# Kernel optimization log

Measured on AMD Instinct MI355X. Metric: run time of the kernel, lower is better.

The kernel has to match this reference:

```python
import jax, jax.numpy as jnp
import numpy as np

ALPHA = 0.01  # LeakyReLU negative slope
NEG_INF = -1e30


def setup_inputs() -> dict:
    key = jax.random.key(0)
    ks = jax.random.split(key, 8)
    B, N, F_IN, F_OUT, H = 4, 512, 256, 128, 64
    x_text = jax.random.normal(ks[0], (B, N, F_IN), dtype=jnp.float32)
    adj = jax.random.randint(ks[1], (B, N, N), 0, 2).astype(jnp.float32)
    # W: Linear(in_features, out_features)
    W = jax.random.normal(ks[2], (F_OUT, F_IN), dtype=jnp.float32) * (1.0 / np.sqrt(F_IN))
    bW = jnp.zeros((F_OUT,), dtype=jnp.float32)
    # afcs: Linear(2*out, hidden) -> ReLU -> Linear(hidden, 1)
    A1 = jax.random.normal(ks[3], (H, 2 * F_OUT), dtype=jnp.float32) * (1.0 / np.sqrt(2 * F_OUT))
    b1 = jnp.zeros((H,), dtype=jnp.float32)
    A2 = jax.random.normal(ks[4], (1, H), dtype=jnp.float32) * (1.0 / np.sqrt(H))
    b2 = jnp.zeros((1,), dtype=jnp.float32)
    return {"x_text": x_text, "adj": adj, "W": W, "bW": bW, "A1": A1, "b1": b1, "A2": A2, "b2": b2}


def reference(x_text, adj, W, bW, A1, b1, A2, b2):
    B, N, _ = x_text.shape
    F_OUT = W.shape[0]
    h = jnp.einsum('bnf,of->bno', x_text, W) + bW  # [B,N,F_OUT]
    # Split first MLP layer: A1 @ concat(h_i, h_j) = A1a h_i + A1b h_j
    A1a, A1b = A1[:, :F_OUT], A1[:, F_OUT:]
    hi = jnp.einsum('bno,ho->bnh', h, A1a)  # contribution of source node i
    hj = jnp.einsum('bno,ho->bnh', h, A1b)  # contribution of target node j
    z = jax.nn.relu(hi[:, :, None, :] + hj[:, None, :, :] + b1)  # [B,N,N,H]
    e = jnp.einsum('bijh,h->bij', z, A2[0]) + b2[0]              # [B,N,N]
    e = jnp.where(e >= 0, e, ALPHA * e)  # LeakyReLU
    logits = e * adj + (1.0 - adj) * NEG_INF  # mask_logits
    # NOTE: original softmax is over the flattened N*N axis per batch element
    attn = jax.nn.softmax(logits.reshape(B, N * N), axis=1).reshape(B, N, N)
    feature = jnp.einsum('bij,bjo->bio', attn, h)  # bmm aggregate
    return jax.nn.elu(feature)  # concat=True
```

## Files before the change

kernel.cpp:

```cpp
#include <hip/hip_runtime.h>
#include <math.h>

#define BB 4
#define NN 512
#define F_IN 256
#define F_OUT 128
#define HH 64
#define NEG_INF_F -1e30f
#define LALPHA 0.01f

typedef float f32x2 __attribute__((ext_vector_type(2)));

__global__ __launch_bounds__(512) void k_proj(
    const float* __restrict__ x, const float* __restrict__ W,
    const float* __restrict__ bW, const float* __restrict__ A1,
    const float* __restrict__ b1,
    float* __restrict__ h, float* __restrict__ hi, float* __restrict__ hjP)
{
    const int row0 = blockIdx.x * 8;
    const int b    = row0 >> 9;
    const int nl0  = row0 & 511;
    const int tid  = threadIdx.x;

    __shared__ float xs[8 * F_IN];
    __shared__ float hs[8 * F_OUT];
    __shared__ float hjs[8 * HH];
    __shared__ float red[4][8][F_OUT];

    #pragma unroll
    for (int t = 0; t < 4; ++t)
        xs[tid + t * 512] = x[(size_t)row0 * F_IN + tid + t * 512];
    __syncthreads();

    {
        const int o  = tid & 127;
        const int kq = tid >> 7;
        float acc[8] = {0, 0, 0, 0, 0, 0, 0, 0};
        const float4* wr = (const float4*)(W + (size_t)o * F_IN + kq * 64);
        #pragma unroll 4
        for (int it = 0; it < 16; ++it) {
            const float4 wv = wr[it];
            #pragma unroll
            for (int r = 0; r < 8; ++r) {
                const float4 xv = *((const float4*)(xs + r * F_IN + kq * 64) + it);
                acc[r] = fmaf(xv.x, wv.x, acc[r]);
                acc[r] = fmaf(xv.y, wv.y, acc[r]);
                acc[r] = fmaf(xv.z, wv.z, acc[r]);
                acc[r] = fmaf(xv.w, wv.w, acc[r]);
            }
        }
        #pragma unroll
        for (int r = 0; r < 8; ++r) red[kq][r][o] = acc[r];
    }
    __syncthreads();
    #pragma unroll
    for (int t = 0; t < 2; ++t) {
        const int idx = tid + t * 512;
        const int r = idx >> 7, o = idx & 127;
        const float v = red[0][r][o] + red[1][r][o] + red[2][r][o] + red[3][r][o] + bW[o];
        h[((size_t)row0 + r) * F_OUT + o] = v;
        hs[r * F_OUT + o] = v;
    }
    __syncthreads();

    {
        const int kh2  = tid & 127;
        const int k    = kh2 & 63, half = kh2 >> 6;
        const int oq   = tid >> 7;
        float acc[8] = {0, 0, 0, 0, 0, 0, 0, 0};
        const float4* ar = (const float4*)(A1 + (size_t)k * (2 * F_OUT) + half * F_OUT + oq * 32);
        #pragma unroll
        for (int it = 0; it < 8; ++it) {
            const float4 av = ar[it];
            #pragma unroll
            for (int r = 0; r < 8; ++r) {
                const float4 hv = *((const float4*)(hs + r * F_OUT + oq * 32) + it);
                acc[r] = fmaf(hv.x, av.x, acc[r]);
                acc[r] = fmaf(hv.y, av.y, acc[r]);
                acc[r] = fmaf(hv.z, av.z, acc[r]);
                acc[r] = fmaf(hv.w, av.w, acc[r]);
            }
        }
        __syncthreads();
        #pragma unroll
        for (int r = 0; r < 8; ++r) red[oq][r][kh2] = acc[r];
    }
    __syncthreads();
    #pragma unroll
    for (int t = 0; t < 2; ++t) {
        const int idx = tid + t * 512;
        const int r = idx >> 7, kh2 = idx & 127;
        const float v = red[0][r][kh2] + red[1][r][kh2] + red[2][r][kh2] + red[3][r][kh2];
        if (kh2 < 64) hi[((size_t)row0 + r) * HH + kh2] = v + b1[kh2];
        else          hjs[r * HH + (kh2 - 64)] = v;
    }
    __syncthreads();
    if (tid < 128) {
        const int k4 = tid >> 3, rr = tid & 7;
        float4 v;
        v.x = hjs[rr * HH + k4 * 4 + 0];
        v.y = hjs[rr * HH + k4 * 4 + 1];
        v.z = hjs[rr * HH + k4 * 4 + 2];
        v.w = hjs[rr * HH + k4 * 4 + 3];
        *(float4*)(hjP + (((size_t)b * 16 + k4) * NN + nl0 + rr) * 4) = v;
    }
}

__global__ __launch_bounds__(512, 2) void k_score_agg(
    const float* __restrict__ hi, const float* __restrict__ hjP,
    const float* __restrict__ A2, const float* __restrict__ b2,
    const float* __restrict__ adj, const float* __restrict__ h,
    float* __restrict__ y, float* __restrict__ stat_m, float* __restrict__ stat_s)
{
    const int blk   = blockIdx.x;
    const int b     = blk >> 7;
    const int itile = (blk >> 1) & 63;
    const int jh    = blk & 1;
    const int i0    = itile * 8;
    const int tid   = threadIdx.x;
    const int jt    = tid & 255;
    const int j     = jh * 256 + jt;

    __shared__ float a2s[HH];
    __shared__ float e_lds[256][12];
    __shared__ float red[4][8][F_OUT];
    __shared__ float rtmp[16];

    if (tid < HH) a2s[tid] = A2[tid];
    __syncthreads();

    float4 hjr[16];
    const float4* hjp = (const float4*)hjP + (size_t)b * 16 * NN + j;
    #pragma unroll
    for (int k4 = 0; k4 < 16; ++k4) hjr[k4] = hjp[(size_t)k4 * NN];

    const int rowu = __builtin_amdgcn_readfirstlane(b * NN + i0 + (tid >> 8) * 4);
    const float* hrow = hi + (size_t)rowu * HH;

    const f32x2 z2 = {0.0f, 0.0f};
    f32x2 s2[4] = {z2, z2, z2, z2};
    #pragma unroll
    for (int k4 = 0; k4 < 16; ++k4) {
        const f32x2 a2lo = *(const f32x2*)(a2s + k4 * 4);
        const f32x2 a2hi = *(const f32x2*)(a2s + k4 * 4 + 2);
        const f32x2 hjlo = {hjr[k4].x, hjr[k4].y};
        const f32x2 hjhi = {hjr[k4].z, hjr[k4].w};
        #pragma unroll
        for (int r = 0; r < 4; ++r) {
            const float* hp = hrow + r * HH + k4 * 4;
            const f32x2 hlo = {hp[0], hp[1]};
            const f32x2 hhi = {hp[2], hp[3]};
            s2[r] = __builtin_elementwise_fma(
                        __builtin_elementwise_max(hlo + hjlo, z2), a2lo, s2[r]);
            s2[r] = __builtin_elementwise_fma(
                        __builtin_elementwise_max(hhi + hjhi, z2), a2hi, s2[r]);
        }
    }
    float s4[4];
    #pragma unroll
    for (int r = 0; r < 4; ++r) s4[r] = s2[r].x + s2[r].y;

    const float b2v = b2[0];
    const int rh = tid >> 8;
    float lmax = -INFINITY;
    #pragma unroll
    for (int r = 0; r < 4; ++r) {
        float v = s4[r] + b2v;
        v = (v >= 0.0f) ? v : LALPHA * v;
        const float a = adj[((size_t)b * NN + i0 + rh * 4 + r) * NN + j];
        v = (a != 0.0f) ? v : NEG_INF_F;
        s4[r] = v;
        lmax = fmaxf(lmax, v);
    }

    #pragma unroll
    for (int off = 32; off; off >>= 1) lmax = fmaxf(lmax, __shfl_xor(lmax, off, 64));
    if ((tid & 63) == 0) rtmp[tid >> 6] = lmax;
    __syncthreads();
    float m_blk = rtmp[0];
    #pragma unroll
    for (int w = 1; w < 8; ++w) m_blk = fmaxf(m_blk, rtmp[w]);

    float4 w4;
    w4.x = __expf(s4[0] - m_blk);
    w4.y = __expf(s4[1] - m_blk);
    w4.z = __expf(s4[2] - m_blk);
    w4.w = __expf(s4[3] - m_blk);
    *(float4*)(&e_lds[jt][rh * 4]) = w4;
    float ls = w4.x + w4.y + w4.z + w4.w;
    #pragma unroll
    for (int off = 32; off; off >>= 1) ls += __shfl_xor(ls, off, 64);
    if ((tid & 63) == 0) rtmp[8 + (tid >> 6)] = ls;
    __syncthreads();
    if (tid == 0) {
        stat_m[blk] = m_blk;
        float ssum = 0.0f;
        #pragma unroll
        for (int w = 0; w < 8; ++w) ssum += rtmp[8 + w];
        stat_s[blk] = ssum;
    }

    {
        const int o = tid & 127;
        const int p = tid >> 7;
        f32x2 acc2[4] = {z2, z2, z2, z2};
        const float* hb = h + (size_t)b * NN * F_OUT;
        #pragma unroll 4
        for (int q = 0; q < 64; ++q) {
            const int jl = p * 64 + q;
            const float hv = hb[(size_t)(jh * 256 + jl) * F_OUT + o];
            const f32x2 hv2 = {hv, hv};
            const f32x2 wa = *(const f32x2*)&e_lds[jl][0];
            const f32x2 wb = *(const f32x2*)&e_lds[jl][2];
            const f32x2 wc = *(const f32x2*)&e_lds[jl][4];
            const f32x2 wd = *(const f32x2*)&e_lds[jl][6];
            acc2[0] = __builtin_elementwise_fma(wa, hv2, acc2[0]);
            acc2[1] = __builtin_elementwise_fma(wb, hv2, acc2[1]);
            acc2[2] = __builtin_elementwise_fma(wc, hv2, acc2[2]);
            acc2[3] = __builtin_elementwise_fma(wd, hv2, acc2[3]);
        }
        #pragma unroll
        for (int c = 0; c < 4; ++c) {
            red[p][2 * c + 0][o] = acc2[c].x;
            red[p][2 * c + 1][o] = acc2[c].y;
        }
    }
    __syncthreads();
    #pragma unroll
    for (int t = 0; t < 2; ++t) {
        const int idx = tid + t * 512;
        const int r = idx >> 7, oo = idx & 127;
        y[(size_t)blk * 1024 + idx] =
            red[0][r][oo] + red[1][r][oo] + red[2][r][oo] + red[3][r][oo];
    }
}

__global__ __launch_bounds__(256) void k_finish(
    const float* __restrict__ y, const float* __restrict__ stat_m,
    const float* __restrict__ stat_s, float* __restrict__ out)
{
    const int blk   = blockIdx.x;
    const int b     = blk >> 6;
    const int itile = blk & 63;
    const int tid   = threadIdx.x;

    __shared__ float sm[4], ss[4];

    const float m = (tid < 128) ? stat_m[b * 128 + tid] : -INFINITY;
    float lm = m;
    #pragma unroll
    for (int off = 32; off; off >>= 1) lm = fmaxf(lm, __shfl_xor(lm, off, 64));
    if ((tid & 63) == 0) sm[tid >> 6] = lm;
    __syncthreads();
    const float M = fmaxf(fmaxf(sm[0], sm[1]), fmaxf(sm[2], sm[3]));

    float sv = (tid < 128) ? stat_s[b * 128 + tid] * expf(m - M) : 0.0f;
    #pragma unroll
    for (int off = 32; off; off >>= 1) sv += __shfl_xor(sv, off, 64);
    if ((tid & 63) == 0) ss[tid >> 6] = sv;
    __syncthreads();
    const float invS = 1.0f / (ss[0] + ss[1] + ss[2] + ss[3]);

    const float sc0 = expf(stat_m[b * 128 + itile * 2 + 0] - M) * invS;
    const float sc1 = expf(stat_m[b * 128 + itile * 2 + 1] - M) * invS;
    const float4* y04 = (const float4*)(y + (size_t)(b * 128 + itile * 2 + 0) * 1024);
    const float4* y14 = (const float4*)(y + (size_t)(b * 128 + itile * 2 + 1) * 1024);
    float4* ob4 = (float4*)(out + ((size_t)b * NN + itile * 8) * F_OUT);

    const float4 v0 = y04[tid];
    const float4 v1 = y14[tid];
    float4 vv;
    vv.x = v0.x * sc0 + v1.x * sc1;
    vv.y = v0.y * sc0 + v1.y * sc1;
    vv.z = v0.z * sc0 + v1.z * sc1;
    vv.w = v0.w * sc0 + v1.w * sc1;
    vv.x = (vv.x > 0.0f) ? vv.x : expm1f(vv.x);
    vv.y = (vv.y > 0.0f) ? vv.y : expm1f(vv.y);
    vv.z = (vv.z > 0.0f) ? vv.z : expm1f(vv.z);
    vv.w = (vv.w > 0.0f) ? vv.w : expm1f(vv.w);
    ob4[tid] = vv;
}

extern "C" void kernel_launch(void* const* d_in, const int* in_sizes, int n_in,
                              void* d_out, int out_size, void* d_ws, size_t ws_size,
                              hipStream_t stream) {
    const float* x   = (const float*)d_in[0];
    const float* adj = (const float*)d_in[1];
    const float* W   = (const float*)d_in[2];
    const float* bW  = (const float*)d_in[3];
    const float* A1  = (const float*)d_in[4];
    const float* b1  = (const float*)d_in[5];
    const float* A2  = (const float*)d_in[6];
    const float* b2  = (const float*)d_in[7];
    float* out = (float*)d_out;

    float* ws = (float*)d_ws;
    float* h      = ws;
    float* hi     = h   + (size_t)BB * NN * F_OUT;
    float* hjP    = hi  + (size_t)BB * NN * HH;
    float* y      = hjP + (size_t)BB * HH * NN;
    float* stat_m = y   + (size_t)512 * 1024;
    float* stat_s = stat_m + 512;

    k_proj     <<<BB * 64,  512, 0, stream>>>(x, W, bW, A1, b1, h, hi, hjP);
    k_score_agg<<<BB * 128, 512, 0, stream>>>(hi, hjP, A2, b2, adj, h, y, stat_m, stat_s);
    k_finish   <<<BB * 64,  256, 0, stream>>>(y, stat_m, stat_s, out);
}
```

Before: 33.47 us.

## Process full j range per score block, halving grid and partial outputs

Each score/aggregate block now covers all 512 target nodes for an 8-row tile instead of splitting j into two halves. Each thread computes 8 rows of scores rather than 4, and aggregation loops over 128 j per group. This halves the partial y buffer and the softmax stats, and simplifies the finish kernel to a single-wave stat reduction with no block syncs. The cost is fewer blocks (256 rather than 512) on a large GPU, more registers per thread and dropped occupancy hint, plus a longer serial aggregation loop.

```diff
diff --git a/kernel.cpp b/kernel.cpp
--- a/kernel.cpp
+++ b/kernel.cpp
@@ -106,23 +106,21 @@
     }
 }
 
-__global__ __launch_bounds__(512, 2) void k_score_agg(
+__global__ __launch_bounds__(512) void k_score_agg(
     const float* __restrict__ hi, const float* __restrict__ hjP,
     const float* __restrict__ A2, const float* __restrict__ b2,
     const float* __restrict__ adj, const float* __restrict__ h,
     float* __restrict__ y, float* __restrict__ stat_m, float* __restrict__ stat_s)
 {
     const int blk   = blockIdx.x;
-    const int b     = blk >> 7;
-    const int itile = (blk >> 1) & 63;
-    const int jh    = blk & 1;
+    const int b     = blk >> 6;
+    const int itile = blk & 63;
     const int i0    = itile * 8;
     const int tid   = threadIdx.x;
-    const int jt    = tid & 255;
-    const int j     = jh * 256 + jt;
+    const int j     = tid;
 
     __shared__ float a2s[HH];
-    __shared__ float e_lds[256][12];
+    __shared__ float e_lds[NN][12];
     __shared__ float red[4][8][F_OUT];
     __shared__ float rtmp[16];
 
@@ -134,11 +132,11 @@
     #pragma unroll
     for (int k4 = 0; k4 < 16; ++k4) hjr[k4] = hjp[(size_t)k4 * NN];
 
-    const int rowu = __builtin_amdgcn_readfirstlane(b * NN + i0 + (tid >> 8) * 4);
+    const int rowu = __builtin_amdgcn_readfirstlane(b * NN + i0);
     const float* hrow = hi + (size_t)rowu * HH;
 
     const f32x2 z2 = {0.0f, 0.0f};
-    f32x2 s2[4] = {z2, z2, z2, z2};
+    f32x2 s2[8] = {z2, z2, z2, z2, z2, z2, z2, z2};
     #pragma unroll
     for (int k4 = 0; k4 < 16; ++k4) {
         const f32x2 a2lo = *(const f32x2*)(a2s + k4 * 4);
@@ -146,7 +144,7 @@
         const f32x2 hjlo = {hjr[k4].x, hjr[k4].y};
         const f32x2 hjhi = {hjr[k4].z, hjr[k4].w};
         #pragma unroll
-        for (int r = 0; r < 4; ++r) {
+        for (int r = 0; r < 8; ++r) {
             const float* hp = hrow + r * HH + k4 * 4;
             const f32x2 hlo = {hp[0], hp[1]};
             const f32x2 hhi = {hp[2], hp[3]};
@@ -156,20 +154,19 @@
                         __builtin_elementwise_max(hhi + hjhi, z2), a2hi, s2[r]);
         }
     }
-    float s4[4];
-    #pragma unroll
-    for (int r = 0; r < 4; ++r) s4[r] = s2[r].x + s2[r].y;
+    float s8[8];
+    #pragma unroll
+    for (int r = 0; r < 8; ++r) s8[r] = s2[r].x + s2[r].y;
 
     const float b2v = b2[0];
-    const int rh = tid >> 8;
     float lmax = -INFINITY;
     #pragma unroll
-    for (int r = 0; r < 4; ++r) {
-        float v = s4[r] + b2v;
+    for (int r = 0; r < 8; ++r) {
+        float v = s8[r] + b2v;
         v = (v >= 0.0f) ? v : LALPHA * v;
-        const float a = adj[((size_t)b * NN + i0 + rh * 4 + r) * NN + j];
+        const float a = adj[((size_t)b * NN + i0 + r) * NN + j];
         v = (a != 0.0f) ? v : NEG_INF_F;
-        s4[r] = v;
+        s8[r] = v;
         lmax = fmaxf(lmax, v);
     }
 
@@ -181,13 +178,18 @@
     #pragma unroll
     for (int w = 1; w < 8; ++w) m_blk = fmaxf(m_blk, rtmp[w]);
 
-    float4 w4;
-    w4.x = __expf(s4[0] - m_blk);
-    w4.y = __expf(s4[1] - m_blk);
-    w4.z = __expf(s4[2] - m_blk);
-    w4.w = __expf(s4[3] - m_blk);
-    *(float4*)(&e_lds[jt][rh * 4]) = w4;
-    float ls = w4.x + w4.y + w4.z + w4.w;
+    float4 wlo, whi;
+    wlo.x = __expf(s8[0] - m_blk);
+    wlo.y = __expf(s8[1] - m_blk);
+    wlo.z = __expf(s8[2] - m_blk);
+    wlo.w = __expf(s8[3] - m_blk);
+    whi.x = __expf(s8[4] - m_blk);
+    whi.y = __expf(s8[5] - m_blk);
+    whi.z = __expf(s8[6] - m_blk);
+    whi.w = __expf(s8[7] - m_blk);
+    *(float4*)(&e_lds[j][0]) = wlo;
+    *(float4*)(&e_lds[j][4]) = whi;
+    float ls = wlo.x + wlo.y + wlo.z + wlo.w + whi.x + whi.y + whi.z + whi.w;
     #pragma unroll
     for (int off = 32; off; off >>= 1) ls += __shfl_xor(ls, off, 64);
     if ((tid & 63) == 0) rtmp[8 + (tid >> 6)] = ls;
@@ -206,9 +208,9 @@
         f32x2 acc2[4] = {z2, z2, z2, z2};
         const float* hb = h + (size_t)b * NN * F_OUT;
         #pragma unroll 4
-        for (int q = 0; q < 64; ++q) {
-            const int jl = p * 64 + q;
-            const float hv = hb[(size_t)(jh * 256 + jl) * F_OUT + o];
+        for (int q = 0; q < 128; ++q) {
+            const int jl = p * 128 + q;
+            const float hv = hb[(size_t)jl * F_OUT + o];
             const f32x2 hv2 = {hv, hv};
             const f32x2 wa = *(const f32x2*)&e_lds[jl][0];
             const f32x2 wb = *(const f32x2*)&e_lds[jl][2];
@@ -244,36 +246,26 @@
     const int itile = blk & 63;
     const int tid   = threadIdx.x;
 
-    __shared__ float sm[4], ss[4];
-
-    const float m = (tid < 128) ? stat_m[b * 128 + tid] : -INFINITY;
+    const int lane = tid & 63;
+    const float m = stat_m[b * 64 + lane];
     float lm = m;
     #pragma unroll
     for (int off = 32; off; off >>= 1) lm = fmaxf(lm, __shfl_xor(lm, off, 64));
-    if ((tid & 63) == 0) sm[tid >> 6] = lm;
-    __syncthreads();
-    const float M = fmaxf(fmaxf(sm[0], sm[1]), fmaxf(sm[2], sm[3]));
-
-    float sv = (tid < 128) ? stat_s[b * 128 + tid] * expf(m - M) : 0.0f;
+    const float M = lm;
+    float sv = stat_s[b * 64 + lane] * __expf(m - M);
     #pragma unroll
     for (int off = 32; off; off >>= 1) sv += __shfl_xor(sv, off, 64);
-    if ((tid & 63) == 0) ss[tid >> 6] = sv;
-    __syncthreads();
-    const float invS = 1.0f / (ss[0] + ss[1] + ss[2] + ss[3]);
-
-    const float sc0 = expf(stat_m[b * 128 + itile * 2 + 0] - M) * invS;
-    const float sc1 = expf(stat_m[b * 128 + itile * 2 + 1] - M) * invS;
-    const float4* y04 = (const float4*)(y + (size_t)(b * 128 + itile * 2 + 0) * 1024);
-    const float4* y14 = (const float4*)(y + (size_t)(b * 128 + itile * 2 + 1) * 1024);
+    const float sc = __expf(stat_m[b * 64 + itile] - M) / sv;
+
+    const float4* y4 = (const float4*)(y + (size_t)blk * 1024);
     float4* ob4 = (float4*)(out + ((size_t)b * NN + itile * 8) * F_OUT);
 
-    const float4 v0 = y04[tid];
-    const float4 v1 = y14[tid];
+    const float4 v0 = y4[tid];
     float4 vv;
-    vv.x = v0.x * sc0 + v1.x * sc1;
-    vv.y = v0.y * sc0 + v1.y * sc1;
-    vv.z = v0.z * sc0 + v1.z * sc1;
-    vv.w = v0.w * sc0 + v1.w * sc1;
+    vv.x = v0.x * sc;
+    vv.y = v0.y * sc;
+    vv.z = v0.z * sc;
+    vv.w = v0.w * sc;
     vv.x = (vv.x > 0.0f) ? vv.x : expm1f(vv.x);
     vv.y = (vv.y > 0.0f) ? vv.y : expm1f(vv.y);
     vv.z = (vv.z > 0.0f) ? vv.z : expm1f(vv.z);
@@ -299,10 +291,10 @@
     float* hi     = h   + (size_t)BB * NN * F_OUT;
     float* hjP    = hi  + (size_t)BB * NN * HH;
     float* y      = hjP + (size_t)BB * HH * NN;
-    float* stat_m = y   + (size_t)512 * 1024;
-    float* stat_s = stat_m + 512;
-
-    k_proj     <<<BB * 64,  512, 0, stream>>>(x, W, bW, A1, b1, h, hi, hjP);
-    k_score_agg<<<BB * 128, 512, 0, stream>>>(hi, hjP, A2, b2, adj, h, y, stat_m, stat_s);
-    k_finish   <<<BB * 64,  256, 0, stream>>>(y, stat_m, stat_s, out);
+    float* stat_m = y   + (size_t)256 * 1024;
+    float* stat_s = stat_m + 256;
+
+    k_proj     <<<BB * 64, 512, 0, stream>>>(x, W, bW, A1, b1, h, hi, hjP);
+    k_score_agg<<<BB * 64, 512, 0, stream>>>(hi, hjP, A2, b2, adj, h, y, stat_m, stat_s);
+    k_finish   <<<BB * 64, 256, 0, stream>>>(y, stat_m, stat_s, out);
 }
```

After: 34.94 us. +4.4%, slower.
